# Performance work log

Measured on AMD Instinct MI355X. Metric: run time of the kernel, lower is better.

The kernel has to match this reference:

```python
import jax, jax.numpy as jnp
import numpy as np
import math

B, S, D, H = 2, 1024, 4096, 32
HD = D // H          # head_dim = 128
P = 10               # prompt_len
THETA = 500000.0     # rope_theta


def _rope(t, cos, sin):
    # t: [b, s, h, hd]; pairs (2i, 2i+1) form complex numbers as in view_as_complex
    tr = t[..., 0::2]
    ti = t[..., 1::2]
    c = cos[None, :, None, :]
    s = sin[None, :, None, :]
    out = jnp.stack([tr * c - ti * s, tr * s + ti * c], axis=-1)  # [b,s,h,hd/2,2]
    return out.reshape(t.shape)


def setup_inputs() -> dict:
    key = jax.random.key(0)
    ks = jax.random.split(key, 8)
    sc = 0.02
    x = jax.random.normal(ks[0], (B, S, D), jnp.float32)
    wq = jax.random.normal(ks[1], (D, D), jnp.float32) * sc
    wk = jax.random.normal(ks[2], (D, D), jnp.float32) * sc
    wv = jax.random.normal(ks[3], (D, D), jnp.float32) * sc
    wo = jax.random.normal(ks[4], (D, D), jnp.float32) * sc
    prompt = jax.random.normal(ks[5], (P, D), jnp.float32)
    prompt_gate = jax.random.normal(ks[6], (1, H, 1, 1), jnp.float32) * 0.1
    # RoPE tables (real/imag of freqs_cis)
    inv = 1.0 / (THETA ** (jnp.arange(0, HD, 2, dtype=jnp.float32) / HD))  # [HD/2]
    ang = jnp.outer(jnp.arange(S, dtype=jnp.float32), inv)                 # [S, HD/2]
    freqs_cos = jnp.cos(ang)
    freqs_sin = jnp.sin(ang)
    # causal additive mask
    mask = jnp.triu(jnp.full((S, S), -1e9, jnp.float32), 1)[None, None]
    type_weight = jax.random.uniform(ks[7], (B, S, 1), jnp.float32)
    return dict(x=x, wq=wq, wk=wk, wv=wv, wo=wo, prompt=prompt,
                prompt_gate=prompt_gate, freqs_cos=freqs_cos,
                freqs_sin=freqs_sin, mask=mask, type_weight=type_weight,
                start_pos=0)


def reference(x, wq, wk, wv, wo, prompt, prompt_gate, freqs_cos, freqs_sin,
              mask, type_weight, start_pos):
    # training-mode forward: start_pos == 0, keys/values = current tokens
    scale = 1.0 / math.sqrt(HD)
    xq = (x @ wq.T).reshape(B, S, H, HD)
    xk = (x @ wk.T).reshape(B, S, H, HD)
    xv = (x @ wv.T).reshape(B, S, H, HD)
    xq = _rope(xq, freqs_cos, freqs_sin)
    xk = _rope(xk, freqs_cos, freqs_sin)
    q = xq.transpose(0, 2, 1, 3)  # [b,h,s,hd]
    k = xk.transpose(0, 2, 1, 3)
    v = xv.transpose(0, 2, 1, 3)
    scores = jnp.einsum('bhqd,bhkd->bhqk', q, k) * scale + mask
    probs = jax.nn.softmax(scores, axis=-1)
    out = jnp.einsum('bhqk,bhkd->bhqd', probs, v)  # [b,h,s,hd]
    # gated prompt injection (num_experts == 1); type_weight unused, as in source
    pk = (prompt @ wk.T).reshape(P, H, HD)
    pv = (prompt @ wv.T).reshape(P, H, HD)
    p_scores = jnp.einsum('bhqd,phd->bhqp', q, pk) * scale
    p_probs = prompt_gate * jax.nn.softmax(p_scores, axis=-1)
    p_out = jnp.einsum('bhqp,phd->bhqd', p_probs, pv)
    out = (out + p_out).transpose(0, 2, 1, 3).reshape(B, S, D)
    return out @ wo.T
```

## Files before the change

### kernel.cpp

```cpp
#include <hip/hip_runtime.h>
#include <hip/hip_bf16.h>
#include <stdint.h>

typedef __hip_bfloat16 bf16;
typedef __attribute__((ext_vector_type(8))) short short8;
typedef __attribute__((ext_vector_type(4))) float f32x4;

#define SCALE_ 0.08838834764831845f

static __device__ __forceinline__ float bf2f(short u) {
  unsigned int x = ((unsigned int)(unsigned short)u) << 16;
  return __builtin_bit_cast(float, x);
}
static __device__ __forceinline__ short f2bf(float f) {
  __hip_bfloat16 h = __float2bfloat16(f);
  return __builtin_bit_cast(short, h);
}
static __device__ __forceinline__ f32x4 mfma16(short8 a, short8 b, f32x4 c) {
  return __builtin_amdgcn_mfma_f32_16x16x32_bf16(a, b, c, 0, 0, 0);
}
static __device__ __forceinline__ void gl_lds16(const bf16* g, bf16* l) {
  __builtin_amdgcn_global_load_lds(
      (const __attribute__((address_space(1))) unsigned int*)g,
      (__attribute__((address_space(3))) unsigned int*)l, 16, 0, 0);
}

__global__ __launch_bounds__(256) void cvt6(
    const float* __restrict__ sx, const float* __restrict__ sq,
    const float* __restrict__ sk, const float* __restrict__ sv,
    const float* __restrict__ so, const float* __restrict__ sp,
    bf16* __restrict__ dx, bf16* __restrict__ dq, bf16* __restrict__ dk,
    bf16* __restrict__ dv, bf16* __restrict__ d4, bf16* __restrict__ dp)
{
  int b = blockIdx.x;
  const float* s; bf16* d; int off;
  if (b < 4096)       { s = sx; d = dx; off = b; }
  else if (b < 12288) { s = sq; d = dq; off = b - 4096; }
  else if (b < 20480) { s = sk; d = dk; off = b - 12288; }
  else if (b < 28672) { s = sv; d = dv; off = b - 20480; }
  else if (b < 36864) { s = so; d = d4; off = b - 28672; }
  else                { s = sp; d = dp; off = b - 36864; }
  long base = (long)off * 2048 + threadIdx.x * 8;
  f32x4 a = *(const f32x4*)(s + base);
  f32x4 c = *(const f32x4*)(s + base + 4);
  short8 o;
#pragma unroll
  for (int j = 0; j < 4; j++) { o[j] = f2bf(a[j]); o[4 + j] = f2bf(c[j]); }
  *(short8*)(d + base) = o;
}

__global__ __launch_bounds__(512, 2) void gemm_bt(
    const bf16* __restrict__ A, const bf16* __restrict__ A2,
    const bf16* __restrict__ B0, const bf16* __restrict__ B1, const bf16* __restrict__ B2w,
    bf16* __restrict__ C0, bf16* __restrict__ C1, bf16* __restrict__ C2,
    bf16* __restrict__ P1, bf16* __restrict__ P2,
    float* __restrict__ CF,
    int M1, int Mtot)
{
  __shared__ char lds[65536];
  const int tid = threadIdx.x, w = tid >> 6, l = tid & 63;
  const int lr = l & 15, lg = l >> 4;
  const int wm = w >> 2, wn = w & 3;
  const int z = blockIdx.z;
  const bf16* Bw = (z == 0) ? B0 : ((z == 1) ? B1 : B2w);
  bf16* C  = (z == 0) ? C0 : ((z == 1) ? C1 : C2);
  bf16* Cp = (z == 0) ? (bf16*)0 : ((z == 1) ? P1 : P2);

  const int cpx = gridDim.x >> 3, orig = blockIdx.x;
  const int wg = (orig & 7) * cpx + (orig >> 3);
  const long m0 = (long)(wg >> 4) * 256;
  const long n0 = (long)(wg & 15) * 256;

  const bf16 *aS0, *aS1, *bS0, *bS1;
  {
    int a0 = w * 64 + l, a1 = 512 + w * 64 + l;
    int r0 = a0 >> 2, r1 = a1 >> 2;
    int c0 = (a0 & 3) ^ ((a0 >> 3) & 3);
    int c1 = (a1 & 3) ^ ((a1 >> 3) & 3);
    long mx = (long)(Mtot - M1) - 1;
    long ra0 = m0 + r0, ra1 = m0 + r1;
    const bf16 *p0, *p1;
    if (ra0 < M1) p0 = A + ra0 * 4096;
    else { long rr = ra0 - M1; if (rr > mx) rr = mx; p0 = A2 + rr * 4096; }
    if (ra1 < M1) p1 = A + ra1 * 4096;
    else { long rr = ra1 - M1; if (rr > mx) rr = mx; p1 = A2 + rr * 4096; }
    aS0 = p0 + c0 * 8;
    aS1 = p1 + c1 * 8;
    bS0 = Bw + (n0 + r0) * 4096 + c0 * 8;
    bS1 = Bw + (n0 + r1) * 4096 + c1 * 8;
  }
  const int fco = (lg ^ ((lr >> 1) & 3)) * 16;
  const int aoffL = (wm * 128 + lr) * 64 + fco;
  const int boffL = 16384 + (wn * 64 + lr) * 64 + fco;

  f32x4 acc[8][4];
#pragma unroll
  for (int i = 0; i < 8; i++)
#pragma unroll
    for (int j = 0; j < 4; j++) acc[i][j] = (f32x4){0.f, 0.f, 0.f, 0.f};

#define G_STAGE(TB_, T_)                                                     \
  {                                                                          \
    gl_lds16(aS0 + (T_) * 32, (bf16*)(lds + (TB_) * 32768 + w * 1024));      \
    gl_lds16(aS1 + (T_) * 32, (bf16*)(lds + (TB_) * 32768 + 8192 + w * 1024)); \
    gl_lds16(bS0 + (T_) * 32, (bf16*)(lds + (TB_) * 32768 + 16384 + w * 1024)); \
    gl_lds16(bS1 + (T_) * 32, (bf16*)(lds + (TB_) * 32768 + 24576 + w * 1024)); \
  }

#define G_ITER(T_, DO_STAGE_)                                                \
  {                                                                          \
    asm volatile("s_waitcnt vmcnt(0)" ::: "memory");                         \
    __builtin_amdgcn_s_barrier();                                            \
    __builtin_amdgcn_sched_barrier(0);                                       \
    if (DO_STAGE_) G_STAGE(((T_) + 1) & 1, (T_) + 1);                        \
    const char* base_ = lds + ((T_) & 1) * 32768;                            \
    short8 af_[8], bf_[4];                                                   \
    _Pragma("unroll") for (int mi = 0; mi < 8; mi++)                         \
      af_[mi] = *(const short8*)(base_ + aoffL + mi * 1024);                 \
    _Pragma("unroll") for (int ni = 0; ni < 4; ni++)                         \
      bf_[ni] = *(const short8*)(base_ + boffL + ni * 1024);                 \
    asm volatile("s_waitcnt lgkmcnt(0)" ::: "memory");                       \
    __builtin_amdgcn_sched_barrier(0);                                       \
    __builtin_amdgcn_s_setprio(1);                                           \
    _Pragma("unroll") for (int mi = 0; mi < 8; mi++)                         \
      _Pragma("unroll") for (int ni = 0; ni < 4; ni++)                       \
        acc[mi][ni] = mfma16(af_[mi], bf_[ni], acc[mi][ni]);                 \
    __builtin_amdgcn_s_setprio(0);                                           \
  }

  G_STAGE(0, 0);
  for (int t = 0; t < 127; ++t)
    G_ITER(t, 1);
  G_ITER(127, 0);

#undef G_ITER
#undef G_STAGE

#pragma unroll
  for (int mi = 0; mi < 8; mi++) {
#pragma unroll
    for (int ni = 0; ni < 4; ni++) {
      long col = n0 + wn * 64 + ni * 16 + lr;
      f32x4 v = acc[mi][ni];
#pragma unroll
      for (int j = 0; j < 4; j++) {
        long row = m0 + wm * 128 + mi * 16 + lg * 4 + j;
        if (CF) {
          CF[row * 4096 + col] = v[j];
        } else if (row < M1) {
          *(short*)(C + row * 4096 + col) = f2bf(v[j]);
        } else if (Cp != 0 && row < Mtot) {
          *(short*)(Cp + (row - M1) * 4096 + col) = f2bf(v[j]);
        }
      }
    }
  }
}

__global__ __launch_bounds__(256) void rope_qk(
    bf16* __restrict__ Q, bf16* __restrict__ Kb,
    const float* __restrict__ FC, const float* __restrict__ FS)
{
  const int row = blockIdx.x;
  const int s = row & 1023;
  const int t = threadIdx.x;
  bf16* base = (blockIdx.y ? Kb : Q) + (long)row * 4096 + t * 16;
  short8 v0 = *(const short8*)base;
  short8 v1 = *(const short8*)(base + 8);
  const float* cp = FC + s * 64 + (t & 7) * 8;
  const float* sp = FS + s * 64 + (t & 7) * 8;
  f32x4 c0 = *(const f32x4*)cp;
  f32x4 c1 = *(const f32x4*)(cp + 4);
  f32x4 s0 = *(const f32x4*)sp;
  f32x4 s1 = *(const f32x4*)(sp + 4);
  short8 o0, o1;
#pragma unroll
  for (int j = 0; j < 4; j++) {
    float c = c0[j], sn = s0[j];
    float e = bf2f(v0[2 * j]), od = bf2f(v0[2 * j + 1]);
    o0[2 * j] = f2bf(e * c - od * sn);
    o0[2 * j + 1] = f2bf(e * sn + od * c);
    float c2 = c1[j], sn2 = s1[j];
    float e2 = bf2f(v1[2 * j]), od2 = bf2f(v1[2 * j + 1]);
    o1[2 * j] = f2bf(e2 * c2 - od2 * sn2);
    o1[2 * j + 1] = f2bf(e2 * sn2 + od2 * c2);
  }
  *(short8*)base = o0;
  *(short8*)(base + 8) = o1;
}

__global__ __launch_bounds__(256) void transpose_v(
    const bf16* __restrict__ V, bf16* __restrict__ VT)
{
  __shared__ bf16 T[64 * 128];
  const int tid = threadIdx.x;
  const int st = blockIdx.x * 64, bh = blockIdx.y;
  const int b = bh >> 5, h = bh & 31;
  const bf16* src = V + ((long)(b * 1024 + st)) * 4096 + h * 128;
#pragma unroll
  for (int rr = 0; rr < 4; ++rr) {
    int i = tid + rr * 256;
    int s_l = i >> 4, c = i & 15;
    short8 v = *(const short8*)(src + (long)s_l * 4096 + c * 8);
    *(short8*)((char*)T + s_l * 256 + ((c ^ (s_l & 7)) * 16)) = v;
  }
  __syncthreads();
#pragma unroll
  for (int rr = 0; rr < 4; ++rr) {
    int i = tid + rr * 256;
    int d = i >> 3, cs = i & 7;
    short8 ov;
#pragma unroll
    for (int e = 0; e < 8; e++) {
      int s_l = cs * 8 + e;
      ov[e] = *(const short*)((char*)T + s_l * 256 + (((d >> 3) ^ (s_l & 7)) * 16) + (d & 7) * 2);
    }
    *(short8*)(VT + ((long)bh * 128 + d) * 1024 + st + cs * 8) = ov;
  }
}

__global__ __launch_bounds__(256) void flash_attn(
    const bf16* __restrict__ Q, const bf16* __restrict__ Kg, const bf16* __restrict__ VT,
    const bf16* __restrict__ PK, const bf16* __restrict__ PV,
    const float* __restrict__ GATE, bf16* __restrict__ O)
{
  __shared__ bf16 Kl[32 * 128];
  __shared__ bf16 Vl[128 * 32];
  __shared__ bf16 PKl[16 * 128];
  __shared__ bf16 PVl[128 * 16];
  __shared__ bf16 Pl[4][16 * 32];
  const int tid = threadIdx.x, w = tid >> 6, l = tid & 63;
  const int lg = l >> 4, lr = l & 15;
  const int qb = blockIdx.x, bh = blockIdx.y;
  const int b = bh >> 5, h = bh & 31;
  const int q0 = qb * 64 + w * 16;

  short8 qf[4];
  {
    const bf16* qp = Q + ((long)(b * 1024 + q0 + lr)) * 4096 + h * 128 + lg * 8;
#pragma unroll
    for (int c = 0; c < 4; c++) qf[c] = *(const short8*)(qp + c * 32);
  }
  {
    int rowp = tid >> 4, pc = tid & 15, lc = pc ^ (rowp & 7);
    short8 v = {0, 0, 0, 0, 0, 0, 0, 0};
    if (rowp < 10) v = *(const short8*)(PK + (long)rowp * 4096 + h * 128 + lc * 8);
    *(short8*)((char*)PKl + tid * 16) = v;
  }
  {
    int d = tid >> 1, pb = (tid & 1) * 8;
#pragma unroll
    for (int e = 0; e < 8; e++) {
      int p = pb + e;
      short v = 0;
      if (p < 10) v = __builtin_bit_cast(short, PV[(long)p * 4096 + h * 128 + d]);
      *(short*)((char*)PVl + d * 32 + (((p >> 3) ^ (d & 1)) * 16) + (p & 7) * 2) = v;
    }
  }
  const float gate = GATE[h];

  f32x4 o[8];
#pragma unroll
  for (int i = 0; i < 8; i++) o[i] = (f32x4){0.f, 0.f, 0.f, 0.f};
  float m_[4] = {-1e30f, -1e30f, -1e30f, -1e30f};
  float l_[4] = {0.f, 0.f, 0.f, 0.f};

  const int nt = (qb + 1) * 2;
  const bf16* Kbase = Kg + ((long)b * 1024) * 4096 + h * 128;
  const bf16* Vbase = VT + ((long)bh) * 128 * 1024;
  const int cb1 = w * 64, cb2 = 256 + w * 64;
  const int iA = cb1 + l, iB = cb2 + l;
  bf16* pw = &Pl[w][0];

  for (int j = 0; j < nt; ++j) {
    __syncthreads();
    {
      const bf16* gA = Kbase + (long)(j * 32 + (iA >> 4)) * 4096 + ((iA & 15) ^ ((iA >> 4) & 7)) * 8;
      const bf16* gB = Kbase + (long)(j * 32 + (iB >> 4)) * 4096 + ((iB & 15) ^ ((iB >> 4) & 7)) * 8;
      gl_lds16(gA, Kl + cb1 * 8);
      gl_lds16(gB, Kl + cb2 * 8);
      const bf16* vA = Vbase + (long)(iA >> 2) * 1024 + j * 32 + ((iA & 3) ^ ((iA >> 2) & 3)) * 8;
      const bf16* vB = Vbase + (long)(iB >> 2) * 1024 + j * 32 + ((iB & 3) ^ ((iB >> 2) & 3)) * 8;
      gl_lds16(vA, Vl + cb1 * 8);
      gl_lds16(vB, Vl + cb2 * 8);
    }
    __syncthreads();

    f32x4 s[2];
#pragma unroll
    for (int ns = 0; ns < 2; ns++) {
      f32x4 a = (f32x4){0.f, 0.f, 0.f, 0.f};
      int krow = ns * 16 + lr;
      const char* kp = (const char*)Kl + krow * 256;
      int sw = krow & 7;
#pragma unroll
      for (int c = 0; c < 4; c++) {
        short8 kf = *(const short8*)(kp + (((c * 4 + lg) ^ sw) * 16));
        a = mfma16(qf[c], kf, a);
      }
      int key = j * 32 + krow;
#pragma unroll
      for (int r = 0; r < 4; r++) {
        int qr = q0 + lg * 4 + r;
        s[ns][r] = a[r] * SCALE_ + ((key <= qr) ? 0.0f : -1e30f);
      }
    }
    float mx[4], cor[4], sum[4];
#pragma unroll
    for (int r = 0; r < 4; r++) mx[r] = fmaxf(s[0][r], s[1][r]);
#pragma unroll
    for (int xm = 1; xm < 16; xm <<= 1)
#pragma unroll
      for (int r = 0; r < 4; r++) mx[r] = fmaxf(mx[r], __shfl_xor(mx[r], xm, 64));
#pragma unroll
    for (int r = 0; r < 4; r++) {
      float mn = fmaxf(m_[r], mx[r]);
      cor[r] = __expf(m_[r] - mn);
      m_[r] = mn;
      s[0][r] = __expf(s[0][r] - mn);
      s[1][r] = __expf(s[1][r] - mn);
      sum[r] = s[0][r] + s[1][r];
    }
#pragma unroll
    for (int xm = 1; xm < 16; xm <<= 1)
#pragma unroll
      for (int r = 0; r < 4; r++) sum[r] += __shfl_xor(sum[r], xm, 64);
#pragma unroll
    for (int r = 0; r < 4; r++) l_[r] = l_[r] * cor[r] + sum[r];
#pragma unroll
    for (int df = 0; df < 8; df++)
#pragma unroll
      for (int r = 0; r < 4; r++) o[df][r] *= cor[r];

#pragma unroll
    for (int ns = 0; ns < 2; ns++)
#pragma unroll
      for (int r = 0; r < 4; r++)
        *(short*)((char*)pw + ((lg * 4 + r) * 32 + ns * 16 + lr) * 2) = f2bf(s[ns][r]);
    asm volatile("s_waitcnt lgkmcnt(0)" ::: "memory");
    __builtin_amdgcn_sched_barrier(0);
    short8 pf = *(const short8*)(pw + lr * 32 + lg * 8);

#pragma unroll
    for (int df = 0; df < 8; df++) {
      int d = df * 16 + lr;
      short8 vf = *(const short8*)((const char*)Vl + d * 64 + ((lg ^ (d & 3)) * 16));
      o[df] = mfma16(pf, vf, o[df]);
    }
  }

  f32x4 ps;
  {
    f32x4 a = (f32x4){0.f, 0.f, 0.f, 0.f};
    const char* kp = (const char*)PKl + lr * 256;
    int sw = lr & 7;
#pragma unroll
    for (int c = 0; c < 4; c++) {
      short8 kf = *(const short8*)(kp + (((c * 4 + lg) ^ sw) * 16));
      a = mfma16(qf[c], kf, a);
    }
#pragma unroll
    for (int r = 0; r < 4; r++) ps[r] = (lr < 10) ? a[r] * SCALE_ : -1e30f;
  }
  {
    float pm[4], pss[4];
#pragma unroll
    for (int r = 0; r < 4; r++) pm[r] = ps[r];
#pragma unroll
    for (int xm = 1; xm < 16; xm <<= 1)
#pragma unroll
      for (int r = 0; r < 4; r++) pm[r] = fmaxf(pm[r], __shfl_xor(pm[r], xm, 64));
#pragma unroll
    for (int r = 0; r < 4; r++) { ps[r] = __expf(ps[r] - pm[r]); pss[r] = ps[r]; }
#pragma unroll
    for (int xm = 1; xm < 16; xm <<= 1)
#pragma unroll
      for (int r = 0; r < 4; r++) pss[r] += __shfl_xor(pss[r], xm, 64);
#pragma unroll
    for (int r = 0; r < 4; r++) ps[r] = ps[r] / pss[r];
  }
#pragma unroll
  for (int r = 0; r < 4; r++) {
    *(short*)((char*)pw + ((lg * 4 + r) * 32 + lr) * 2) = f2bf(ps[r]);
    *(short*)((char*)pw + ((lg * 4 + r) * 32 + 16 + lr) * 2) = 0;
  }
  asm volatile("s_waitcnt lgkmcnt(0)" ::: "memory");
  __builtin_amdgcn_sched_barrier(0);
  short8 pf2 = *(const short8*)(pw + lr * 32 + lg * 8);
  f32x4 po[8];
#pragma unroll
  for (int df = 0; df < 8; df++) {
    int d = df * 16 + lr;
    short8 vf = {0, 0, 0, 0, 0, 0, 0, 0};
    if (lg < 2) vf = *(const short8*)((const char*)PVl + d * 32 + ((lg ^ (d & 1)) * 16));
    po[df] = mfma16(pf2, vf, (f32x4){0.f, 0.f, 0.f, 0.f});
  }

  bf16* op = O + ((long)(b * 1024 + q0 + lg * 4)) * 4096 + h * 128 + lr;
#pragma unroll
  for (int df = 0; df < 8; df++)
#pragma unroll
    for (int r = 0; r < 4; r++) {
      float val = o[df][r] / l_[r] + gate * po[df][r];
      *(short*)(op + (long)r * 4096 + df * 16) = f2bf(val);
    }
}

extern "C" void kernel_launch(void* const* d_in, const int* in_sizes, int n_in,
                              void* d_out, int out_size, void* d_ws, size_t ws_size,
                              hipStream_t stream) {
  (void)in_sizes; (void)n_in; (void)out_size; (void)ws_size;
  const float* x      = (const float*)d_in[0];
  const float* wq     = (const float*)d_in[1];
  const float* wk     = (const float*)d_in[2];
  const float* wv     = (const float*)d_in[3];
  const float* wo     = (const float*)d_in[4];
  const float* prompt = (const float*)d_in[5];
  const float* gate   = (const float*)d_in[6];
  const float* fcos   = (const float*)d_in[7];
  const float* fsin   = (const float*)d_in[8];
  float* out = (float*)d_out;
  char* ws = (char*)d_ws;

  size_t o = 0;
  bf16* xb  = (bf16*)(ws + o); o += (size_t)8388608 * 2;
  bf16* wqb = (bf16*)(ws + o); o += (size_t)16777216 * 2;
  bf16* wkb = (bf16*)(ws + o); o += (size_t)16777216 * 2;
  bf16* wvb = (bf16*)(ws + o); o += (size_t)16777216 * 2;
  bf16* wob = (bf16*)(ws + o); o += (size_t)16777216 * 2;
  bf16* pb  = (bf16*)(ws + o); o += (size_t)40960 * 2;
  bf16* q_ws  = (bf16*)(ws + o); o += (size_t)2048 * 4096 * 2;
  bf16* k_ws  = (bf16*)(ws + o); o += (size_t)2048 * 4096 * 2;
  bf16* v_ws  = (bf16*)(ws + o); o += (size_t)2048 * 4096 * 2;
  bf16* vT_ws = (bf16*)(ws + o); o += (size_t)2048 * 4096 * 2;
  bf16* pk_ws = (bf16*)(ws + o); o += (size_t)40960 * 2;
  bf16* pv_ws = (bf16*)(ws + o); o += (size_t)40960 * 2;
  bf16* attn_ws = v_ws;

  cvt6<<<dim3(36884), 256, 0, stream>>>(x, wq, wk, wv, wo, prompt,
                                        xb, wqb, wkb, wvb, wob, pb);
  gemm_bt<<<dim3(144, 1, 3), 512, 0, stream>>>(
      xb, pb, wqb, wkb, wvb, q_ws, k_ws, v_ws, pk_ws, pv_ws, (float*)0, 2048, 2058);
  rope_qk<<<dim3(2048, 2), 256, 0, stream>>>(q_ws, k_ws, fcos, fsin);
  transpose_v<<<dim3(16, 64), 256, 0, stream>>>(v_ws, vT_ws);
  flash_attn<<<dim3(16, 64), 256, 0, stream>>>(
      q_ws, k_ws, vT_ws, pk_ws, pv_ws, gate, attn_ws);
  gemm_bt<<<dim3(128, 1, 1), 512, 0, stream>>>(
      attn_ws, (const bf16*)0, wob, wob, wob, q_ws, q_ws, q_ws,
      (bf16*)0, (bf16*)0, out, 2048, 2048);
}
```

Baseline: 566.4 us.

## Deepen GEMM global-to-LDS pipeline from double to four-stage buffering

The bf16 GEMM now keeps four LDS stages instead of two and prefetches three K-tiles ahead. Partial vmcnt waits replace the full drain before each iteration, so global loads for later tiles can stay in flight while MFMAs run. The cost is doubling the static LDS to 128 KB per block, which likely allows only one 512-thread block per CU instead of two and reduces latency hiding from co-resident blocks.

```diff
diff --git a/kernel.cpp b/kernel.cpp
--- a/kernel.cpp
+++ b/kernel.cpp
@@ -57,7 +57,7 @@
     float* __restrict__ CF,
     int M1, int Mtot)
 {
-  __shared__ char lds[65536];
+  __shared__ char lds[131072];
   const int tid = threadIdx.x, w = tid >> 6, l = tid & 63;
   const int lr = l & 15, lg = l >> 4;
   const int wm = w >> 2, wn = w & 3;
@@ -99,41 +99,50 @@
 #pragma unroll
     for (int j = 0; j < 4; j++) acc[i][j] = (f32x4){0.f, 0.f, 0.f, 0.f};
 
-#define G_STAGE(TB_, T_)                                                     \
-  {                                                                          \
-    gl_lds16(aS0 + (T_) * 32, (bf16*)(lds + (TB_) * 32768 + w * 1024));      \
-    gl_lds16(aS1 + (T_) * 32, (bf16*)(lds + (TB_) * 32768 + 8192 + w * 1024)); \
-    gl_lds16(bS0 + (T_) * 32, (bf16*)(lds + (TB_) * 32768 + 16384 + w * 1024)); \
-    gl_lds16(bS1 + (T_) * 32, (bf16*)(lds + (TB_) * 32768 + 24576 + w * 1024)); \
-  }
-
-#define G_ITER(T_, DO_STAGE_)                                                \
-  {                                                                          \
-    asm volatile("s_waitcnt vmcnt(0)" ::: "memory");                         \
-    __builtin_amdgcn_s_barrier();                                            \
-    __builtin_amdgcn_sched_barrier(0);                                       \
-    if (DO_STAGE_) G_STAGE(((T_) + 1) & 1, (T_) + 1);                        \
-    const char* base_ = lds + ((T_) & 1) * 32768;                            \
-    short8 af_[8], bf_[4];                                                   \
-    _Pragma("unroll") for (int mi = 0; mi < 8; mi++)                         \
-      af_[mi] = *(const short8*)(base_ + aoffL + mi * 1024);                 \
-    _Pragma("unroll") for (int ni = 0; ni < 4; ni++)                         \
-      bf_[ni] = *(const short8*)(base_ + boffL + ni * 1024);                 \
-    asm volatile("s_waitcnt lgkmcnt(0)" ::: "memory");                       \
-    __builtin_amdgcn_sched_barrier(0);                                       \
-    __builtin_amdgcn_s_setprio(1);                                           \
-    _Pragma("unroll") for (int mi = 0; mi < 8; mi++)                         \
-      _Pragma("unroll") for (int ni = 0; ni < 4; ni++)                       \
-        acc[mi][ni] = mfma16(af_[mi], bf_[ni], acc[mi][ni]);                 \
-    __builtin_amdgcn_s_setprio(0);                                           \
+#define G_STAGE(TB_, T_)                                                       \
+  {                                                                            \
+    char* bb_ = lds + (TB_) * 32768;                                           \
+    gl_lds16(aS0 + (T_) * 32, (bf16*)(bb_ + w * 1024));                        \
+    gl_lds16(aS1 + (T_) * 32, (bf16*)(bb_ + 8192 + w * 1024));                 \
+    gl_lds16(bS0 + (T_) * 32, (bf16*)(bb_ + 16384 + w * 1024));                \
+    gl_lds16(bS1 + (T_) * 32, (bf16*)(bb_ + 24576 + w * 1024));                \
+  }
+
+#define G_BODY(T_, DO_STAGE_)                                                  \
+  {                                                                            \
+    __builtin_amdgcn_s_barrier();                                              \
+    __builtin_amdgcn_sched_barrier(0);                                         \
+    if (DO_STAGE_) G_STAGE(((T_) + 3) & 3, (T_) + 3);                          \
+    const char* base_ = lds + (((T_) & 3) * 32768);                            \
+    short8 af_[8], bf_[4];                                                     \
+    _Pragma("unroll") for (int mi = 0; mi < 8; mi++)                           \
+      af_[mi] = *(const short8*)(base_ + aoffL + mi * 1024);                   \
+    _Pragma("unroll") for (int ni = 0; ni < 4; ni++)                           \
+      bf_[ni] = *(const short8*)(base_ + boffL + ni * 1024);                   \
+    asm volatile("s_waitcnt lgkmcnt(0)" ::: "memory");                         \
+    __builtin_amdgcn_sched_barrier(0);                                         \
+    __builtin_amdgcn_s_setprio(1);                                             \
+    _Pragma("unroll") for (int mi = 0; mi < 8; mi++)                           \
+      _Pragma("unroll") for (int ni = 0; ni < 4; ni++)                         \
+        acc[mi][ni] = mfma16(af_[mi], bf_[ni], acc[mi][ni]);                   \
+    __builtin_amdgcn_s_setprio(0);                                             \
   }
 
   G_STAGE(0, 0);
-  for (int t = 0; t < 127; ++t)
-    G_ITER(t, 1);
-  G_ITER(127, 0);
-
-#undef G_ITER
+  G_STAGE(1, 1);
+  G_STAGE(2, 2);
+  for (int t = 0; t < 125; ++t) {
+    asm volatile("s_waitcnt vmcnt(8)" ::: "memory");
+    G_BODY(t, 1);
+  }
+  asm volatile("s_waitcnt vmcnt(8)" ::: "memory");
+  G_BODY(125, 0);
+  asm volatile("s_waitcnt vmcnt(4)" ::: "memory");
+  G_BODY(126, 0);
+  asm volatile("s_waitcnt vmcnt(0)" ::: "memory");
+  G_BODY(127, 0);
+
+#undef G_BODY
 #undef G_STAGE
 
 #pragma unroll
```

After: 544.9 us. 1.04x faster.

## Deepen GEMM LDS pipeline with 64-wide K tiles and split-phase staging

Applied to the files above, without the earlier changes.

Doubles LDS to 128KB and reorganizes the bf16 GEMM main loop into 64-wide K tiles, each split into four phases. Each phase issues one slice of the next tile's global-to-LDS loads and waits only on partial vmcnt. MFMA work is split into half-M chunks, which reduces live fragment registers and lets loads overlap compute more finely. The new LDS layout and swizzle change the address maps. The larger LDS footprint also lowers how many blocks can be resident per CU, against the launch bound of 2.

```diff
diff --git a/kernel.cpp b/kernel.cpp
--- a/kernel.cpp
+++ b/kernel.cpp
@@ -57,7 +57,7 @@
     float* __restrict__ CF,
     int M1, int Mtot)
 {
-  __shared__ char lds[65536];
+  __shared__ char lds[131072];
   const int tid = threadIdx.x, w = tid >> 6, l = tid & 63;
   const int lr = l & 15, lg = l >> 4;
   const int wm = w >> 2, wn = w & 3;
@@ -71,27 +71,26 @@
   const long m0 = (long)(wg >> 4) * 256;
   const long n0 = (long)(wg & 15) * 256;
 
-  const bf16 *aS0, *aS1, *bS0, *bS1;
-  {
-    int a0 = w * 64 + l, a1 = 512 + w * 64 + l;
-    int r0 = a0 >> 2, r1 = a1 >> 2;
-    int c0 = (a0 & 3) ^ ((a0 >> 3) & 3);
-    int c1 = (a1 & 3) ^ ((a1 >> 3) & 3);
+  const int r0 = ((tid >> 3) << 1) | ((tid >> 2) & 1);
+  const int c0 = (tid & 3) ^ ((tid >> 3) & 3);
+  const bf16 *pa0, *pa1;
+  {
     long mx = (long)(Mtot - M1) - 1;
-    long ra0 = m0 + r0, ra1 = m0 + r1;
-    const bf16 *p0, *p1;
-    if (ra0 < M1) p0 = A + ra0 * 4096;
-    else { long rr = ra0 - M1; if (rr > mx) rr = mx; p0 = A2 + rr * 4096; }
-    if (ra1 < M1) p1 = A + ra1 * 4096;
-    else { long rr = ra1 - M1; if (rr > mx) rr = mx; p1 = A2 + rr * 4096; }
-    aS0 = p0 + c0 * 8;
-    aS1 = p1 + c1 * 8;
-    bS0 = Bw + (n0 + r0) * 4096 + c0 * 8;
-    bS1 = Bw + (n0 + r1) * 4096 + c1 * 8;
-  }
-  const int fco = (lg ^ ((lr >> 1) & 3)) * 16;
-  const int aoffL = (wm * 128 + lr) * 64 + fco;
-  const int boffL = 16384 + (wn * 64 + lr) * 64 + fco;
+    long g0 = m0 + r0, g1 = m0 + r0 + 128;
+    const bf16 *q0, *q1;
+    if (g0 < M1) q0 = A + g0 * 4096;
+    else { long rr = g0 - M1; if (rr > mx) rr = mx; q0 = A2 + rr * 4096; }
+    if (g1 < M1) q1 = A + g1 * 4096;
+    else { long rr = g1 - M1; if (rr > mx) rr = mx; q1 = A2 + rr * 4096; }
+    pa0 = q0 + c0 * 8;
+    pa1 = q1 + c0 * 8;
+  }
+  const bf16* pb0 = Bw + (n0 + r0) * 4096 + c0 * 8;
+  const bf16* pb1 = pb0 + (long)128 * 4096;
+
+  const int ro  = (lr >> 1) * 128 + (((lr & 1) * 4) + (lg ^ ((lr >> 1) & 3))) * 16;
+  const int aro = wm * 8192 + ro;
+  const int bro = wn * 4096 + ro;
 
   f32x4 acc[8][4];
 #pragma unroll
@@ -99,42 +98,68 @@
 #pragma unroll
     for (int j = 0; j < 4; j++) acc[i][j] = (f32x4){0.f, 0.f, 0.f, 0.f};
 
-#define G_STAGE(TB_, T_)                                                     \
+  short8 af[4], bf[4];
+
+#define STG(PSB_, J_, P0_, P1_, KE_)                                         \
   {                                                                          \
-    gl_lds16(aS0 + (T_) * 32, (bf16*)(lds + (TB_) * 32768 + w * 1024));      \
-    gl_lds16(aS1 + (T_) * 32, (bf16*)(lds + (TB_) * 32768 + 8192 + w * 1024)); \
-    gl_lds16(bS0 + (T_) * 32, (bf16*)(lds + (TB_) * 32768 + 16384 + w * 1024)); \
-    gl_lds16(bS1 + (T_) * 32, (bf16*)(lds + (TB_) * 32768 + 24576 + w * 1024)); \
-  }
-
-#define G_ITER(T_, DO_STAGE_)                                                \
+    bf16* d_ = (bf16*)(lds + (PSB_) + (J_) * 16384) + tid * 8;               \
+    gl_lds16((P0_) + (KE_), d_);                                             \
+    gl_lds16((P1_) + (KE_), d_ + 4096);                                      \
+  }
+
+#define PHASE(VMS_, PRB_, AU_, BU_, MO_, LB_, STGC_)                         \
   {                                                                          \
-    asm volatile("s_waitcnt vmcnt(0)" ::: "memory");                         \
+    asm volatile("s_waitcnt vmcnt(" VMS_ ")" ::: "memory");                  \
     __builtin_amdgcn_s_barrier();                                            \
     __builtin_amdgcn_sched_barrier(0);                                       \
-    if (DO_STAGE_) G_STAGE(((T_) + 1) & 1, (T_) + 1);                        \
-    const char* base_ = lds + ((T_) & 1) * 32768;                            \
-    short8 af_[8], bf_[4];                                                   \
-    _Pragma("unroll") for (int mi = 0; mi < 8; mi++)                         \
-      af_[mi] = *(const short8*)(base_ + aoffL + mi * 1024);                 \
-    _Pragma("unroll") for (int ni = 0; ni < 4; ni++)                         \
-      bf_[ni] = *(const short8*)(base_ + boffL + ni * 1024);                 \
+    STGC_                                                                    \
+    const char* ab_ = lds + (PRB_) + (AU_) + aro;                            \
+    _Pragma("unroll") for (int mi = 0; mi < 4; mi++)                         \
+      af[mi] = *(const short8*)(ab_ + ((MO_) + mi) * 1024);                  \
+    if (LB_) {                                                               \
+      const char* bb_ = lds + (PRB_) + (BU_) + bro;                          \
+      _Pragma("unroll") for (int ni = 0; ni < 4; ni++)                       \
+        bf[ni] = *(const short8*)(bb_ + ni * 1024);                          \
+    }                                                                        \
     asm volatile("s_waitcnt lgkmcnt(0)" ::: "memory");                       \
     __builtin_amdgcn_sched_barrier(0);                                       \
     __builtin_amdgcn_s_setprio(1);                                           \
-    _Pragma("unroll") for (int mi = 0; mi < 8; mi++)                         \
+    _Pragma("unroll") for (int mi = 0; mi < 4; mi++)                         \
       _Pragma("unroll") for (int ni = 0; ni < 4; ni++)                       \
-        acc[mi][ni] = mfma16(af_[mi], bf_[ni], acc[mi][ni]);                 \
+        acc[(MO_) + mi][ni] = mfma16(af[mi], bf[ni], acc[(MO_) + mi][ni]);   \
     __builtin_amdgcn_s_setprio(0);                                           \
   }
 
-  G_STAGE(0, 0);
-  for (int t = 0; t < 127; ++t)
-    G_ITER(t, 1);
-  G_ITER(127, 0);
-
-#undef G_ITER
-#undef G_STAGE
+#define KTILE(PRB_, PSB_, KE_)                                               \
+  PHASE("4", PRB_, 0,     16384, 0, 1, STG(PSB_, 0, pa0, pa1, (KE_)))        \
+  PHASE("4", PRB_, 0,     16384, 4, 0, STG(PSB_, 1, pb0, pb1, (KE_)))        \
+  PHASE("4", PRB_, 32768, 49152, 0, 1, STG(PSB_, 2, pa0, pa1, (KE_) + 32))   \
+  PHASE("4", PRB_, 32768, 49152, 4, 0, STG(PSB_, 3, pb0, pb1, (KE_) + 32))
+
+#define KTILE_LAST(PRB_)                                                     \
+  PHASE("4", PRB_, 0,     16384, 0, 1, )                                     \
+  PHASE("4", PRB_, 0,     16384, 4, 0, )                                     \
+  PHASE("0", PRB_, 32768, 49152, 0, 1, )                                     \
+  PHASE("0", PRB_, 32768, 49152, 4, 0, )
+
+  STG(0, 0, pa0, pa1, 0)
+  STG(0, 1, pb0, pb1, 0)
+  STG(0, 2, pa0, pa1, 32)
+  STG(0, 3, pb0, pb1, 32)
+
+  for (int kt = 0; kt < 62; kt += 2) {
+    const int ke1 = (kt + 1) * 64;
+    const int ke2 = (kt + 2) * 64;
+    KTILE(0, 65536, ke1)
+    KTILE(65536, 0, ke2)
+  }
+  KTILE(0, 65536, 4032)
+  KTILE_LAST(65536)
+
+#undef KTILE_LAST
+#undef KTILE
+#undef PHASE
+#undef STG
 
 #pragma unroll
   for (int mi = 0; mi < 8; mi++) {
```

New measurement: 530.5 us. -6.4%, faster.
